# Performance work log

Hardware: AMD Instinct MI355X
Metric: run time of the kernel (lower is better)

The kernel has to match this reference:

```python
import jax, jax.numpy as jnp
import numpy as np
from jax import lax

EPS = 1e-8


def setup_inputs() -> dict:
    key = jax.random.key(0)
    k1, k2, k3, k4, k5 = jax.random.split(key, 5)
    b, c_in, c_out, h, w_sp, k, z = 8, 256, 256, 128, 128, 3, 512
    return {
        "x": jax.random.normal(k1, (b, c_in, h, w_sp), dtype=jnp.float32),
        "w": jax.random.normal(k2, (b, z), dtype=jnp.float32),
        "weight": jax.random.normal(k3, (c_out, c_in, k, k), dtype=jnp.float32),
        "affine_w": jax.random.normal(k4, (c_in, z), dtype=jnp.float32) * 0.02,
        "affine_b": jax.random.normal(k5, (c_in,), dtype=jnp.float32) * 0.02,
    }


def reference(x, w, weight, affine_w, affine_b):
    # style: [b, c_in] -> broadcast over (out_ch, kh, kw); +1 as in StyleGAN2
    style = w @ affine_w.T + affine_b + 1.0                      # [b, c_in]
    wgt = weight[None] * style[:, None, :, None, None]           # [b, O, I, kh, kw]
    # demodulation
    denom = lax.rsqrt(jnp.sum(wgt * wgt, axis=(2, 3, 4)) + EPS)  # [b, O]
    wgt = wgt * denom[:, :, None, None, None]

    # per-sample conv (equivalent to groups=b grouped conv), 'same' padding
    def conv_one(xi, wi):
        # xi: [I, H, W], wi: [O, I, kh, kw]
        return lax.conv_general_dilated(
            xi[None], wi, window_strides=(1, 1), padding="SAME",
            dimension_numbers=("NCHW", "OIHW", "NCHW"))[0]

    return jax.vmap(conv_one)(x, wgt)                            # [b, O, H, W]
```

## Files before the change

kernel.cpp:

```cpp
#include <hip/hip_runtime.h>
#include <hip/hip_bf16.h>

#define EPS 1e-8f

using short8 = __attribute__((ext_vector_type(8))) short;
using f32x16 = __attribute__((ext_vector_type(16))) float;
typedef unsigned short u16;

#define BARRIER() do { __builtin_amdgcn_s_barrier(); \
                       asm volatile("" ::: "memory"); } while (0)
#define LGKM0() asm volatile("s_waitcnt lgkmcnt(0)" ::: "memory")

__device__ __forceinline__ u16 f2bf(float f) {
    union { float f; unsigned u; } v; v.f = f;
    unsigned u = v.u;
    return (u16)((u + 0x7FFFu + ((u >> 16) & 1u)) >> 16);
}

__global__ void style_kernel(const float* __restrict__ w,
                             const float* __restrict__ affine_w,
                             const float* __restrict__ affine_b,
                             float* __restrict__ style) {
    int b = blockIdx.x;
    int i = threadIdx.x;
    __shared__ float wb[512];
    for (int z = threadIdx.x; z < 512; z += 256) wb[z] = w[b * 512 + z];
    __syncthreads();
    const float* aw = affine_w + i * 512;
    float acc = 0.f;
#pragma unroll 4
    for (int z = 0; z < 512; z += 4) {
        float4 a4 = *reinterpret_cast<const float4*>(aw + z);
        acc += a4.x * wb[z] + a4.y * wb[z + 1] + a4.z * wb[z + 2] + a4.w * wb[z + 3];
    }
    style[b * 256 + i] = acc + affine_b[i] + 1.0f;
}

__global__ void modw_kernel(const float* __restrict__ weight,
                            const float* __restrict__ style,
                            u16* __restrict__ wgt) {
    int b = blockIdx.x >> 8;
    int o = blockIdx.x & 255;
    int ic = threadIdx.x;
    float s = style[b * 256 + ic];
    const float* wp = weight + (size_t)(o * 256 + ic) * 9;
    float m[9];
    float ss = 0.f;
#pragma unroll
    for (int t = 0; t < 9; ++t) { m[t] = wp[t] * s; ss += m[t] * m[t]; }
#pragma unroll
    for (int off = 32; off > 0; off >>= 1) ss += __shfl_down(ss, off);
    __shared__ float part[4];
    int lane = threadIdx.x & 63, wid = threadIdx.x >> 6;
    if (lane == 0) part[wid] = ss;
    __syncthreads();
    float denom = rsqrtf(part[0] + part[1] + part[2] + part[3] + EPS);
    int g = ic >> 3, j = ic & 7;
#pragma unroll
    for (int t = 0; t < 9; ++t) {
        size_t idx = ((((size_t)(b * 9 + t) * 32 + g) * 256 + o) << 3) + j;
        wgt[idx] = f2bf(m[t] * denom);
    }
}

__global__ __launch_bounds__(256, 2) void conv_kernel(
    const float* __restrict__ x,
    const u16* __restrict__ wgt,
    float* __restrict__ out) {

    __shared__ __align__(16) u16 Xs[2][4][4][130][8];

    int bid = blockIdx.x;
    int swz = (bid & 7) * 128 + (bid >> 3);
    int ht = swz & 63, ot = (swz >> 6) & 1, b = swz >> 7;
    int h0 = ht * 2;

    int tid = threadIdx.x, lane = tid & 63, wid = tid >> 6;
    int wm = wid >> 1, wr = wid & 1;
    int l31 = lane & 31, lh = lane >> 5;
    int lw = lane & 31, hi = lane >> 5;
    int jbase = hi * 4;
    int koff = hi * 2;

    int hr = h0 + wid - 1;
    bool hValid = ((unsigned)hr < 128u);
    int hc = hValid ? hr : 0;

    const u16* aBase = wgt + ((size_t)(b * 9) * 32 * 256 +
                              (size_t)(lh * 256 + ot * 128 + wm * 64 + l31)) * 8;
    const float* xSt = x + (((size_t)(b * 256 + jbase)) * 128 + hc) * 128 + 4 * lw;

    auto loadA = [&](short8 dst[2][2], int c, int t) {
#pragma unroll
        for (int kk = 0; kk < 2; ++kk)
#pragma unroll
            for (int mi = 0; mi < 2; ++mi)
                dst[kk][mi] = *reinterpret_cast<const short8*>(
                    aBase + (size_t)(((t * 32) + c * 4 + kk * 2) * 256 + mi * 32) * 8);
    };
    auto issueX = [&](float* dst, int c1, int g) {
        const float* sp = xSt + (size_t)(c1 * 32 + g * 8) * 16384;
#pragma unroll
        for (int i = 0; i < 4; ++i)
            *reinterpret_cast<float4*>(&dst[i * 4]) =
                *reinterpret_cast<const float4*>(sp + (size_t)i * 16384);
    };
    auto writeX = [&](const float* src, int g, int bx) {
        unsigned X[4][2];
#pragma unroll
        for (int k = 0; k < 4; ++k)
#pragma unroll
            for (int d = 0; d < 2; ++d) {
                __hip_bfloat16 b0 = __float2bfloat16(src[(2 * d) * 4 + k]);
                __hip_bfloat16 b1 = __float2bfloat16(src[(2 * d + 1) * 4 + k]);
                X[k][d] = (unsigned)reinterpret_cast<u16&>(b0) |
                          ((unsigned)reinterpret_cast<u16&>(b1) << 16);
            }
        unsigned a00 = X[0][0], c00 = X[2][0];
        unsigned a01 = X[0][1], c01 = X[2][1];
        unsigned a10 = X[1][0], c10 = X[3][0];
        unsigned a11 = X[1][1], c11 = X[3][1];
        asm volatile("v_permlane32_swap_b32 %0, %1" : "+v"(a00), "+v"(c00));
        asm volatile("v_permlane32_swap_b32 %0, %1" : "+v"(a01), "+v"(c01));
        asm volatile("v_permlane32_swap_b32 %0, %1" : "+v"(a10), "+v"(c10));
        asm volatile("v_permlane32_swap_b32 %0, %1" : "+v"(a11), "+v"(c11));
        union { unsigned d[4]; short8 v; } oA, oB;
        oA.d[0] = a00; oA.d[1] = a01; oA.d[2] = c00; oA.d[3] = c01;
        oB.d[0] = a10; oB.d[1] = a11; oB.d[2] = c10; oB.d[3] = c11;
        int slotA = 1 + 4 * lw + koff;
        *reinterpret_cast<short8*>(&Xs[bx][wid][g][slotA][0])     = oA.v;
        *reinterpret_cast<short8*>(&Xs[bx][wid][g][slotA + 1][0]) = oB.v;
    };

    {
        short8 z = {0, 0, 0, 0, 0, 0, 0, 0};
        short8* p0 = reinterpret_cast<short8*>(&Xs[0][0][0][0][0]);
        for (int i = tid; i < 4160; i += 256) p0[i] = z;
    }
    __syncthreads();

    short8 afC[2][2], afN[2][2];
    if (hValid) {
        float xg0[16];
#pragma unroll
        for (int g = 0; g < 4; ++g) { issueX(xg0, 0, g); writeX(xg0, g, 0); }
    }
    loadA(afC, 0, 0);
    LGKM0();
    BARRIER();

    f32x16 acc[2][4] = {};
    float xg[16];

    for (int c = 0; c < 8; ++c) {
        int buf = c & 1;
        bool stage = (c < 7) && hValid;
#pragma unroll
        for (int t = 0; t < 9; ++t) {
            bool lastTap = (c == 7 && t == 8);
            if (!lastTap)
                loadA(afN, t < 8 ? c : c + 1, t < 8 ? t + 1 : 0);
            if (stage) {
                if (t >= 1 && t < 5) writeX(xg, t - 1, buf ^ 1);
                if (t < 4)           issueX(xg, c + 1, t);
            }

            int kh = t / 3, kw = t - kh * 3;
            short8 bx8[2][4];
#pragma unroll
            for (int kk = 0; kk < 2; ++kk)
#pragma unroll
                for (int ni = 0; ni < 4; ++ni)
                    bx8[kk][ni] = *reinterpret_cast<const short8*>(
                        &Xs[buf][wr + kh][kk * 2 + lh][ni * 32 + l31 + kw][0]);
            __builtin_amdgcn_s_setprio(1);
#pragma unroll
            for (int mi = 0; mi < 2; ++mi)
#pragma unroll
                for (int ni = 0; ni < 4; ++ni)
#pragma unroll
                    for (int kk = 0; kk < 2; ++kk)
                        acc[mi][ni] = __builtin_amdgcn_mfma_f32_32x32x16_bf16(
                            afC[kk][mi], bx8[kk][ni], acc[mi][ni], 0, 0, 0);
            __builtin_amdgcn_s_setprio(0);

            if (!lastTap) {
#pragma unroll
                for (int k2 = 0; k2 < 2; ++k2)
#pragma unroll
                    for (int mi = 0; mi < 2; ++mi)
                        afC[k2][mi] = afN[k2][mi];
            }
        }
        if (c < 7) { LGKM0(); BARRIER(); }
    }

    int h = h0 + wr;
#pragma unroll
    for (int mi = 0; mi < 2; ++mi) {
        int ob = ot * 128 + wm * 64 + mi * 32 + 4 * lh;
#pragma unroll
        for (int ni = 0; ni < 4; ++ni) {
            int w_ = ni * 32 + l31;
#pragma unroll
            for (int reg = 0; reg < 16; ++reg) {
                int o = ob + (reg & 3) + 8 * (reg >> 2);
                out[(((size_t)(b * 256 + o) * 128 + h) * 128) + w_] = acc[mi][ni][reg];
            }
        }
    }
}

extern "C" void kernel_launch(void* const* d_in, const int* in_sizes, int n_in,
                              void* d_out, int out_size, void* d_ws, size_t ws_size,
                              hipStream_t stream) {
    const float* x        = (const float*)d_in[0];
    const float* w        = (const float*)d_in[1];
    const float* weight   = (const float*)d_in[2];
    const float* affine_w = (const float*)d_in[3];
    const float* affine_b = (const float*)d_in[4];
    float* out = (float*)d_out;

    float* style = (float*)d_ws;
    u16* wgt = (u16*)((char*)d_ws + 8192);

    style_kernel<<<8, 256, 0, stream>>>(w, affine_w, affine_b, style);
    modw_kernel<<<2048, 256, 0, stream>>>(weight, style, wgt);
    conv_kernel<<<1024, 256, 0, stream>>>(x, wgt, out);
}
```

Before: 173.6 us.

## Shrink conv tile to one output row per block for higher occupancy

Each conv block now computes a single output row instead of two, with the four waves splitting the 128 output channels by 128 width columns (2x2 MFMA tiles per wave instead of 2x4). The halo buffer shrinks from 4 to 3 input rows, cutting LDS use, and launch bounds rise to 3 blocks per CU across twice as many blocks. The A-fragment double-buffer is dropped in favour of loading directly each tap. The cost is that each input row is now staged by three blocks instead of two, adding more redundant global loads of x, and the weight loads are no longer prefetched one tap ahead.

```diff
diff --git a/kernel.cpp b/kernel.cpp
--- a/kernel.cpp
+++ b/kernel.cpp
@@ -63,145 +63,140 @@
     }
 }
 
-__global__ __launch_bounds__(256, 2) void conv_kernel(
+__global__ __launch_bounds__(256, 3) void conv_kernel(
     const float* __restrict__ x,
     const u16* __restrict__ wgt,
     float* __restrict__ out) {
 
-    __shared__ __align__(16) u16 Xs[2][4][4][130][8];
+    __shared__ __align__(16) u16 Xs[2][3][4][130][8];
 
     int bid = blockIdx.x;
-    int swz = (bid & 7) * 128 + (bid >> 3);
-    int ht = swz & 63, ot = (swz >> 6) & 1, b = swz >> 7;
-    int h0 = ht * 2;
+    int swz = (bid & 7) * 256 + (bid >> 3);
+    int h = swz & 127, ot = (swz >> 7) & 1, b = swz >> 8;
 
     int tid = threadIdx.x, lane = tid & 63, wid = tid >> 6;
-    int wm = wid >> 1, wr = wid & 1;
+    int wm = wid >> 1, wn = wid & 1;
     int l31 = lane & 31, lh = lane >> 5;
-    int lw = lane & 31, hi = lane >> 5;
+    int lw = l31, hi = lh;
     int jbase = hi * 4;
     int koff = hi * 2;
 
-    int hr = h0 + wid - 1;
-    bool hValid = ((unsigned)hr < 128u);
-    int hc = hValid ? hr : 0;
-
-    const u16* aBase = wgt + ((size_t)(b * 9) * 32 * 256 +
-                              (size_t)(lh * 256 + ot * 128 + wm * 64 + l31)) * 8;
-    const float* xSt = x + (((size_t)(b * 256 + jbase)) * 128 + hc) * 128 + 4 * lw;
+    const u16* aLane = wgt + (size_t)(lh * 256 + ot * 128 + wm * 64 + l31) * 8;
 
     auto loadA = [&](short8 dst[2][2], int c, int t) {
+        const u16* p = aLane + (size_t)((b * 9 + t) * 32 + c * 4) * 2048;
 #pragma unroll
         for (int kk = 0; kk < 2; ++kk)
 #pragma unroll
             for (int mi = 0; mi < 2; ++mi)
                 dst[kk][mi] = *reinterpret_cast<const short8*>(
-                    aBase + (size_t)(((t * 32) + c * 4 + kk * 2) * 256 + mi * 32) * 8);
+                    p + kk * 2 * 2048 + mi * 256);
     };
-    auto issueX = [&](float* dst, int c1, int g) {
-        const float* sp = xSt + (size_t)(c1 * 32 + g * 8) * 16384;
-#pragma unroll
-        for (int i = 0; i < 4; ++i)
-            *reinterpret_cast<float4*>(&dst[i * 4]) =
-                *reinterpret_cast<const float4*>(sp + (size_t)i * 16384);
+    auto issueX = [&](float* dst, int c1, int u) {
+        int row = u >> 2, g = u & 3;
+        int hr = h + row - 1;
+        if ((unsigned)hr < 128u) {
+            const float* sp = x + (((size_t)(b * 256 + c1 * 32 + g * 8 + jbase)) * 128 + hr) * 128 + 4 * lw;
+#pragma unroll
+            for (int i = 0; i < 4; ++i)
+                *reinterpret_cast<float4*>(&dst[i * 4]) =
+                    *reinterpret_cast<const float4*>(sp + (size_t)i * 16384);
+        }
     };
-    auto writeX = [&](const float* src, int g, int bx) {
-        unsigned X[4][2];
-#pragma unroll
-        for (int k = 0; k < 4; ++k)
-#pragma unroll
-            for (int d = 0; d < 2; ++d) {
-                __hip_bfloat16 b0 = __float2bfloat16(src[(2 * d) * 4 + k]);
-                __hip_bfloat16 b1 = __float2bfloat16(src[(2 * d + 1) * 4 + k]);
-                X[k][d] = (unsigned)reinterpret_cast<u16&>(b0) |
-                          ((unsigned)reinterpret_cast<u16&>(b1) << 16);
-            }
-        unsigned a00 = X[0][0], c00 = X[2][0];
-        unsigned a01 = X[0][1], c01 = X[2][1];
-        unsigned a10 = X[1][0], c10 = X[3][0];
-        unsigned a11 = X[1][1], c11 = X[3][1];
-        asm volatile("v_permlane32_swap_b32 %0, %1" : "+v"(a00), "+v"(c00));
-        asm volatile("v_permlane32_swap_b32 %0, %1" : "+v"(a01), "+v"(c01));
-        asm volatile("v_permlane32_swap_b32 %0, %1" : "+v"(a10), "+v"(c10));
-        asm volatile("v_permlane32_swap_b32 %0, %1" : "+v"(a11), "+v"(c11));
-        union { unsigned d[4]; short8 v; } oA, oB;
-        oA.d[0] = a00; oA.d[1] = a01; oA.d[2] = c00; oA.d[3] = c01;
-        oB.d[0] = a10; oB.d[1] = a11; oB.d[2] = c10; oB.d[3] = c11;
-        int slotA = 1 + 4 * lw + koff;
-        *reinterpret_cast<short8*>(&Xs[bx][wid][g][slotA][0])     = oA.v;
-        *reinterpret_cast<short8*>(&Xs[bx][wid][g][slotA + 1][0]) = oB.v;
+    auto writeX = [&](const float* src, int u, int bx) {
+        int row = u >> 2, g = u & 3;
+        int hr = h + row - 1;
+        if ((unsigned)hr < 128u) {
+            unsigned X[4][2];
+#pragma unroll
+            for (int k = 0; k < 4; ++k)
+#pragma unroll
+                for (int d = 0; d < 2; ++d) {
+                    __hip_bfloat16 b0 = __float2bfloat16(src[(2 * d) * 4 + k]);
+                    __hip_bfloat16 b1 = __float2bfloat16(src[(2 * d + 1) * 4 + k]);
+                    X[k][d] = (unsigned)reinterpret_cast<u16&>(b0) |
+                              ((unsigned)reinterpret_cast<u16&>(b1) << 16);
+                }
+            unsigned a00 = X[0][0], c00 = X[2][0];
+            unsigned a01 = X[0][1], c01 = X[2][1];
+            unsigned a10 = X[1][0], c10 = X[3][0];
+            unsigned a11 = X[1][1], c11 = X[3][1];
+            asm volatile("v_permlane32_swap_b32 %0, %1" : "+v"(a00), "+v"(c00));
+            asm volatile("v_permlane32_swap_b32 %0, %1" : "+v"(a01), "+v"(c01));
+            asm volatile("v_permlane32_swap_b32 %0, %1" : "+v"(a10), "+v"(c10));
+            asm volatile("v_permlane32_swap_b32 %0, %1" : "+v"(a11), "+v"(c11));
+            union { unsigned d[4]; short8 v; } oA, oB;
+            oA.d[0] = a00; oA.d[1] = a01; oA.d[2] = c00; oA.d[3] = c01;
+            oB.d[0] = a10; oB.d[1] = a11; oB.d[2] = c10; oB.d[3] = c11;
+            int slotA = 1 + 4 * lw + koff;
+            *reinterpret_cast<short8*>(&Xs[bx][row][g][slotA][0])     = oA.v;
+            *reinterpret_cast<short8*>(&Xs[bx][row][g][slotA + 1][0]) = oB.v;
+        }
     };
 
     {
         short8 z = {0, 0, 0, 0, 0, 0, 0, 0};
         short8* p0 = reinterpret_cast<short8*>(&Xs[0][0][0][0][0]);
-        for (int i = tid; i < 4160; i += 256) p0[i] = z;
+        for (int i = tid; i < 3120; i += 256) p0[i] = z;
     }
     __syncthreads();
 
-    short8 afC[2][2], afN[2][2];
-    if (hValid) {
-        float xg0[16];
-#pragma unroll
-        for (int g = 0; g < 4; ++g) { issueX(xg0, 0, g); writeX(xg0, g, 0); }
-    }
-    loadA(afC, 0, 0);
+    {
+        float xa[16], xc[16];
+        int u0 = wid * 3;
+        issueX(xa, 0, u0);
+        issueX(xc, 0, u0 + 1);
+        writeX(xa, u0, 0);
+        issueX(xa, 0, u0 + 2);
+        writeX(xc, u0 + 1, 0);
+        writeX(xa, u0 + 2, 0);
+    }
     LGKM0();
     BARRIER();
 
-    f32x16 acc[2][4] = {};
+    f32x16 acc[2][2] = {};
+    short8 afC[2][2];
     float xg[16];
 
     for (int c = 0; c < 8; ++c) {
         int buf = c & 1;
-        bool stage = (c < 7) && hValid;
+        bool stage = (c < 7);
 #pragma unroll
         for (int t = 0; t < 9; ++t) {
-            bool lastTap = (c == 7 && t == 8);
-            if (!lastTap)
-                loadA(afN, t < 8 ? c : c + 1, t < 8 ? t + 1 : 0);
+            loadA(afC, c, t);
             if (stage) {
-                if (t >= 1 && t < 5) writeX(xg, t - 1, buf ^ 1);
-                if (t < 4)           issueX(xg, c + 1, t);
+                if (t >= 1 && t < 4) writeX(xg, wid * 3 + (t - 1), buf ^ 1);
+                if (t < 3)           issueX(xg, c + 1, wid * 3 + t);
             }
 
             int kh = t / 3, kw = t - kh * 3;
-            short8 bx8[2][4];
+            short8 bx2[2][2];
 #pragma unroll
             for (int kk = 0; kk < 2; ++kk)
 #pragma unroll
-                for (int ni = 0; ni < 4; ++ni)
-                    bx8[kk][ni] = *reinterpret_cast<const short8*>(
-                        &Xs[buf][wr + kh][kk * 2 + lh][ni * 32 + l31 + kw][0]);
+                for (int ni = 0; ni < 2; ++ni)
+                    bx2[kk][ni] = *reinterpret_cast<const short8*>(
+                        &Xs[buf][kh][kk * 2 + lh][wn * 64 + ni * 32 + l31 + kw][0]);
             __builtin_amdgcn_s_setprio(1);
 #pragma unroll
             for (int mi = 0; mi < 2; ++mi)
 #pragma unroll
-                for (int ni = 0; ni < 4; ++ni)
+                for (int ni = 0; ni < 2; ++ni)
 #pragma unroll
                     for (int kk = 0; kk < 2; ++kk)
                         acc[mi][ni] = __builtin_amdgcn_mfma_f32_32x32x16_bf16(
-                            afC[kk][mi], bx8[kk][ni], acc[mi][ni], 0, 0, 0);
+                            afC[kk][mi], bx2[kk][ni], acc[mi][ni], 0, 0, 0);
             __builtin_amdgcn_s_setprio(0);
-
-            if (!lastTap) {
-#pragma unroll
-                for (int k2 = 0; k2 < 2; ++k2)
-#pragma unroll
-                    for (int mi = 0; mi < 2; ++mi)
-                        afC[k2][mi] = afN[k2][mi];
-            }
         }
         if (c < 7) { LGKM0(); BARRIER(); }
     }
 
-    int h = h0 + wr;
 #pragma unroll
     for (int mi = 0; mi < 2; ++mi) {
         int ob = ot * 128 + wm * 64 + mi * 32 + 4 * lh;
 #pragma unroll
-        for (int ni = 0; ni < 4; ++ni) {
-            int w_ = ni * 32 + l31;
+        for (int ni = 0; ni < 2; ++ni) {
+            int w_ = wn * 64 + ni * 32 + l31;
 #pragma unroll
             for (int reg = 0; reg < 16; ++reg) {
                 int o = ob + (reg & 3) + 8 * (reg >> 2);
@@ -226,5 +221,5 @@
 
     style_kernel<<<8, 256, 0, stream>>>(w, affine_w, affine_b, style);
     modw_kernel<<<2048, 256, 0, stream>>>(weight, style, wgt);
-    conv_kernel<<<1024, 256, 0, stream>>>(x, wgt, out);
-}
+    conv_kernel<<<2048, 256, 0, stream>>>(x, wgt, out);
+}
```

Result: slower. 197.6 us (+13.8%).
